# Optimization experiments

Hardware: AMD Instinct MI355X
Metric: run time of the kernel (lower is better)

Reference implementation:

```python
import jax, jax.numpy as jnp
import numpy as np

HASH_CODE_LEN = 8  # config['hash_code_len']
EPS = 1e-12

def _l2norm(x):
    n = jnp.sqrt(jnp.sum(x * x, axis=-1, keepdims=True))
    return x / jnp.maximum(n, EPS)

def setup_inputs() -> dict:
    key = jax.random.key(0)
    k1, k2, k3, k4 = jax.random.split(key, 4)
    B, H, S, D = 2, 12, 2048, 64
    Q = jax.random.normal(k1, (B, H, S, D), dtype=jnp.float32)
    K = jax.random.normal(k2, (B, H, S, D), dtype=jnp.float32)
    V = jax.random.normal(k3, (B, H, S, D), dtype=jnp.float32)
    mask = jnp.ones((B, S), dtype=jnp.float32)
    conv_w = jax.random.normal(k4, (H, 1, 3, 1), dtype=jnp.float32)  # depthwise Conv2d weight [H,1,w,1]
    return {"Q": Q, "K": K, "V": V, "mask": mask, "conv_w": conv_w}

def reference(Q, K, V, mask, conv_w):
    B, H, S, D = Q.shape
    # conv branch: depthwise conv over the sequence axis, per head (groups=num_head)
    Vm = V * mask[:, None, :, None]  # [B,H,S,D]
    conv_V = jax.lax.conv_general_dilated(
        Vm, conv_w,
        window_strides=(1, 1),
        padding=[(1, 1), (0, 0)],  # (conv_window//2, 0)
        dimension_numbers=("NCHW", "OIHW", "NCHW"),
        feature_group_count=H,
    )
    # YOSO attention: exact expectation of LSH cumulation.
    # collision prob of unit vectors q,k over hash_code_len bits: (1 - acos(q.k)/pi)^tau
    qn = _l2norm(Q)
    kn = _l2norm(K)
    dots = jnp.einsum("bhsd,bhtd->bhst", qn, kn)
    dots = jnp.clip(dots, -1.0, 1.0)
    W = (1.0 - jnp.arccos(dots) / jnp.pi) ** HASH_CODE_LEN  # [B,H,S,S]
    W = W * mask[:, None, None, :]  # key mask
    X = jnp.einsum("bhst,bhtd->bhsd", W, V)
    X = X * mask[:, None, :, None]  # query mask
    X = _l2norm(X)  # kernel.normalize(X)
    return X + conv_V
```

## Files before the change

### kernel.cpp

```cpp
#include <hip/hip_runtime.h>
#include <hip/hip_bf16.h>
#include <math.h>

#define NB 2
#define NH 12
#define NS 2048
#define ND 64
#define NBH (NB * NH)
#define TILE_USHORT 4096
#define QK_BLOCKS 6144
#define V_BLOCKS (NBH * 32)

typedef __attribute__((ext_vector_type(8))) short short8;
typedef __attribute__((ext_vector_type(4))) float floatx4;
typedef __attribute__((ext_vector_type(2))) float float2v;

__device__ __forceinline__ unsigned short f32_to_bf16_rne(float f) {
  unsigned int u = __float_as_uint(f);
  u += 0x7fffu + ((u >> 16) & 1u);
  return (unsigned short)(u >> 16);
}

__device__ __forceinline__ unsigned int pack_bf16_trunc(float lo, float hi) {
  return __builtin_amdgcn_perm(__float_as_uint(hi), __float_as_uint(lo), 0x07060302);
}

__device__ __forceinline__ float2v mk2(float x) { return (float2v){x, x}; }
__device__ __forceinline__ float2v max2(float2v a, float2v b) {
  return (float2v){fmaxf(a[0], b[0]), fmaxf(a[1], b[1])};
}
__device__ __forceinline__ float2v abs2(float2v a) {
  return (float2v){fabsf(a[0]), fabsf(a[1])};
}

__device__ __forceinline__ float yoso_f_exact(float d) {
  const float c0 = 0.49996030f;
  const float c1 = -0.06751822f;
  const float c2 = 0.02363774f;
  const float c3 = -0.00596174f;
  float a = fminf(fabsf(d), 1.0f);
  float p = fmaf(fmaf(fmaf(c3, a, c2), a, c1), a, c0);
  float u = sqrtf(1.0f - a) * p;
  return (d >= 0.0f) ? (1.0f - u) : u;
}

__global__ __launch_bounds__(256) void prep_all(
    const float* __restrict__ Q, const float* __restrict__ K,
    const float* __restrict__ V, const float* __restrict__ mask,
    unsigned short* __restrict__ qimg, unsigned short* __restrict__ kimg,
    unsigned short* __restrict__ vimg) {
  int blk = blockIdx.x;
  if (blk < QK_BLOCKS) {
    int row = blk * 16 + (threadIdx.x >> 4);
    int li  = threadIdx.x & 15;
    const float* src = Q;
    unsigned short* dst = qimg;
    if (row >= NBH * NS) { src = K; dst = kimg; row -= NBH * NS; }
    float4 v = *(const float4*)(src + (size_t)row * ND + li * 4);
    float ss = v.x * v.x + v.y * v.y + v.z * v.z + v.w * v.w;
    ss += __shfl_xor(ss, 1, 64);
    ss += __shfl_xor(ss, 2, 64);
    ss += __shfl_xor(ss, 4, 64);
    ss += __shfl_xor(ss, 8, 64);
    float rn = 1.0f / fmaxf(sqrtf(ss), 1e-12f);
    ushort4 o;
    o.x = f32_to_bf16_rne(v.x * rn);
    o.y = f32_to_bf16_rne(v.y * rn);
    o.z = f32_to_bf16_rne(v.z * rn);
    o.w = f32_to_bf16_rne(v.w * rn);
    int bh = row >> 11;
    int s  = row & (NS - 1);
    int kt = s >> 6, r = s & 63;
    int frag = (li >> 3) * 4 + (r >> 4);
    int ln   = ((li >> 1) & 3) * 16 + (r & 15);
    size_t off = (size_t)(bh * 32 + kt) * TILE_USHORT + frag * 512 + ln * 8 + (li & 1) * 4;
    *(ushort4*)(dst + off) = o;
  } else {
    int vb = blk - QK_BLOCKS;
    int bh = vb >> 5, kt = vb & 31, t0 = kt * 64;
    int b  = bh / NH;
    __shared__ float sT[64][65];
    int tid = threadIdx.x;
    int tr = tid >> 2;
    int dc = (tid & 3) * 16;
    float m = mask[b * NS + t0 + tr];
    const float* vp = V + ((size_t)bh * NS + t0 + tr) * ND + dc;
    #pragma unroll
    for (int jj = 0; jj < 16; jj += 4) {
      float4 v = *(const float4*)(vp + jj);
      sT[dc + jj + 0][tr] = v.x * m;
      sT[dc + jj + 1][tr] = v.y * m;
      sT[dc + jj + 2][tr] = v.z * m;
      sT[dc + jj + 3][tr] = v.w * m;
    }
    __syncthreads();
    int dr = tid >> 2;
    unsigned short* op = vimg + (size_t)(bh * 32 + kt) * TILE_USHORT;
    #pragma unroll
    for (int g = 0; g < 2; ++g) {
      int combo = (tid & 3) * 2 + g;
      int kk2 = combo >> 2;
      int qd  = combo & 3;
      uint4 u;
      int tb = kk2 * 32 + qd * 4;
      u.x = (unsigned int)f32_to_bf16_rne(sT[dr][tb + 0]) |
            ((unsigned int)f32_to_bf16_rne(sT[dr][tb + 1]) << 16);
      u.y = (unsigned int)f32_to_bf16_rne(sT[dr][tb + 2]) |
            ((unsigned int)f32_to_bf16_rne(sT[dr][tb + 3]) << 16);
      u.z = (unsigned int)f32_to_bf16_rne(sT[dr][tb + 16]) |
            ((unsigned int)f32_to_bf16_rne(sT[dr][tb + 17]) << 16);
      u.w = (unsigned int)f32_to_bf16_rne(sT[dr][tb + 18]) |
            ((unsigned int)f32_to_bf16_rne(sT[dr][tb + 19]) << 16);
      int frag = kk2 * 4 + (dr >> 4);
      int ln   = qd * 16 + (dr & 15);
      *(uint4*)(op + frag * 512 + ln * 8) = u;
    }
  }
}

__global__ __launch_bounds__(256, 3) void yoso_main(
    const unsigned short* __restrict__ qimg, const unsigned short* __restrict__ kimg,
    const unsigned short* __restrict__ vimg, const float* __restrict__ V,
    const float* __restrict__ mask, const float* __restrict__ conv_w,
    float* __restrict__ out) {
  int bh = blockIdx.x >> 5;
  int b  = bh / NH;
  int h  = bh % NH;
  int qt = blockIdx.x & 31;
  int s0 = qt * 64;

  __shared__ float xch[4 * 1088];

  int tid  = threadIdx.x;
  int wv   = tid >> 6;
  int lane = tid & 63;
  int lq   = lane & 15;
  int quad = lane >> 4;
  int qh   = wv & 1;
  int kp   = wv >> 1;

  uint4 qfrag[2][2];
  {
    const unsigned short* qtile = qimg + (size_t)(bh * 32 + qt) * TILE_USHORT;
    #pragma unroll
    for (int su = 0; su < 2; ++su)
      #pragma unroll
      for (int kk = 0; kk < 2; ++kk)
        qfrag[su][kk] = *(const uint4*)(qtile + (kk * 4 + qh * 2 + su) * 512 + lane * 8);
  }

  float w0 = conv_w[h * 3 + 0], w1 = conv_w[h * 3 + 1], w2 = conv_w[h * 3 + 2];

  floatx4 acc[2][4];
  #pragma unroll
  for (int su = 0; su < 2; ++su)
    #pragma unroll
    for (int fd = 0; fd < 4; ++fd) acc[su][fd] = (floatx4){0.f, 0.f, 0.f, 0.f};

  const unsigned short* kb  = kimg + (size_t)bh * 32 * TILE_USHORT;
  const unsigned short* vbI = vimg + (size_t)bh * 32 * TILE_USHORT;

  const float P0 = 0.3183098862f;
  const float P1 = 0.0530516477f;
  const float P2 = 0.0238732415f;
  const float P3 = 0.0142098402f;
  const float P4 = 0.0096701727f;
  const float P5 = 0.0071212906f;

  #pragma unroll 1
  for (int ss = 0; ss < 16; ++ss) {
    int kt = ss * 2 + kp;
    const unsigned short* ktile = kb  + (size_t)kt * TILE_USHORT;
    const unsigned short* vtile = vbI + (size_t)kt * TILE_USHORT;

    uint4 kf[2][4];
    #pragma unroll
    for (int kk = 0; kk < 2; ++kk)
      #pragma unroll
      for (int ft = 0; ft < 4; ++ft)
        kf[kk][ft] = *(const uint4*)(ktile + (kk * 4 + ft) * 512 + lane * 8);

    floatx4 sc[2][4];
    #pragma unroll
    for (int su = 0; su < 2; ++su)
      #pragma unroll
      for (int ft = 0; ft < 4; ++ft) sc[su][ft] = (floatx4){0.f, 0.f, 0.f, 0.f};
    #pragma unroll
    for (int kk = 0; kk < 2; ++kk)
      #pragma unroll
      for (int su = 0; su < 2; ++su) {
        short8 bq = *(const short8*)&qfrag[su][kk];
        #pragma unroll
        for (int ft = 0; ft < 4; ++ft)
          sc[su][ft] = __builtin_amdgcn_mfma_f32_16x16x32_bf16(
              *(const short8*)&kf[kk][ft], bq, sc[su][ft], 0, 0, 0);
      }

    uint4 vf[2][4];
    #pragma unroll
    for (int kk2 = 0; kk2 < 2; ++kk2)
      #pragma unroll
      for (int fd = 0; fd < 4; ++fd)
        vf[kk2][fd] = *(const uint4*)(vtile + (kk2 * 4 + fd) * 512 + lane * 8);

    {
      float2v mxy = mk2(0.f);
      #pragma unroll
      for (int su = 0; su < 2; ++su)
        #pragma unroll
        for (int ft = 0; ft < 4; ++ft) {
          float2v* p = (float2v*)&sc[su][ft];
          mxy = max2(mxy, max2(abs2(p[0]), abs2(p[1])));
        }
      float mx = fmaxf(mxy[0], mxy[1]);
      if (__builtin_expect(__any(mx > 0.82f), 0)) {
        #pragma unroll
        for (int su = 0; su < 2; ++su)
          #pragma unroll
          for (int ft = 0; ft < 4; ++ft)
            #pragma unroll
            for (int r = 0; r < 4; ++r) {
              float f = yoso_f_exact(sc[su][ft][r]);
              float f2 = f * f;
              float f4 = f2 * f2;
              sc[su][ft][r] = f4 * f4;
            }
      } else {
        float2v c5 = mk2(P5), c4 = mk2(P4), c3 = mk2(P3), c2 = mk2(P2),
                c1 = mk2(P1), c0 = mk2(P0), hf = mk2(0.5f);
        #pragma unroll
        for (int su = 0; su < 2; ++su)
          #pragma unroll
          for (int ft = 0; ft < 4; ++ft) {
            float2v* p = (float2v*)&sc[su][ft];
            #pragma unroll
            for (int hh = 0; hh < 2; ++hh) {
              float2v d = p[hh];
              float2v y = d * d;
              float2v pp = ((((c5 * y + c4) * y + c3) * y + c2) * y + c1) * y + c0;
              float2v f = pp * d + hf;
              float2v f2 = f * f;
              float2v f4 = f2 * f2;
              p[hh] = f4 * f4;
            }
          }
      }
    }

    #pragma unroll
    for (int kk2 = 0; kk2 < 2; ++kk2)
      #pragma unroll
      for (int su = 0; su < 2; ++su) {
        uint4 u;
        u.x = pack_bf16_trunc(sc[su][2 * kk2][0], sc[su][2 * kk2][1]);
        u.y = pack_bf16_trunc(sc[su][2 * kk2][2], sc[su][2 * kk2][3]);
        u.z = pack_bf16_trunc(sc[su][2 * kk2 + 1][0], sc[su][2 * kk2 + 1][1]);
        u.w = pack_bf16_trunc(sc[su][2 * kk2 + 1][2], sc[su][2 * kk2 + 1][3]);
        short8 bw = *(short8*)&u;
        #pragma unroll
        for (int fd = 0; fd < 4; ++fd)
          acc[su][fd] = __builtin_amdgcn_mfma_f32_16x16x32_bf16(
              *(const short8*)&vf[kk2][fd], bw, acc[su][fd], 0, 0, 0);
      }
  }

  __syncthreads();
  {
    float* wr = xch + wv * 1088;
    #pragma unroll
    for (int fd = 0; fd < 4; ++fd)
      #pragma unroll
      for (int r = 0; r < 4; ++r)
        wr[lq * 68 + fd * 16 + quad * 4 + r] = acc[1 - kp][fd][r];
  }
  __syncthreads();
  {
    const float* rd = xch + (wv ^ 2) * 1088;
    #pragma unroll
    for (int fd = 0; fd < 4; ++fd)
      #pragma unroll
      for (int r = 0; r < 4; ++r)
        acc[kp][fd][r] += rd[lq * 68 + fd * 16 + quad * 4 + r];
  }

  int s = s0 + qh * 32 + kp * 16 + lq;
  float qm  = mask[b * NS + s];
  float qm0 = (s > 0) ? mask[b * NS + s - 1] : 0.f;
  float qm2 = (s < NS - 1) ? mask[b * NS + s + 1] : 0.f;
  float ssum = 0.f;
  #pragma unroll
  for (int fd = 0; fd < 4; ++fd)
    #pragma unroll
    for (int r = 0; r < 4; ++r) {
      float x = acc[kp][fd][r] * qm;
      acc[kp][fd][r] = x;
      ssum += x * x;
    }
  ssum += __shfl_xor(ssum, 16, 64);
  ssum += __shfl_xor(ssum, 32, 64);
  float rn = 1.0f / fmaxf(sqrtf(ssum), 1e-12f);

  const float* vfull = V + ((size_t)bh * NS + s) * ND;
  #pragma unroll
  for (int fd = 0; fd < 4; ++fd) {
    int d = fd * 16 + quad * 4;
    float4 vc1 = *(const float4*)(vfull + d);
    float4 cv;
    cv.x = w1 * vc1.x * qm; cv.y = w1 * vc1.y * qm;
    cv.z = w1 * vc1.z * qm; cv.w = w1 * vc1.w * qm;
    if (s > 0) {
      float4 vc0 = *(const float4*)(vfull - ND + d);
      cv.x += w0 * vc0.x * qm0; cv.y += w0 * vc0.y * qm0;
      cv.z += w0 * vc0.z * qm0; cv.w += w0 * vc0.w * qm0;
    }
    if (s < NS - 1) {
      float4 vc2 = *(const float4*)(vfull + ND + d);
      cv.x += w2 * vc2.x * qm2; cv.y += w2 * vc2.y * qm2;
      cv.z += w2 * vc2.z * qm2; cv.w += w2 * vc2.w * qm2;
    }
    float4 o;
    o.x = acc[kp][fd][0] * rn + cv.x;
    o.y = acc[kp][fd][1] * rn + cv.y;
    o.z = acc[kp][fd][2] * rn + cv.z;
    o.w = acc[kp][fd][3] * rn + cv.w;
    *(float4*)(out + ((size_t)bh * NS + s) * ND + d) = o;
  }
}

extern "C" void kernel_launch(void* const* d_in, const int* in_sizes, int n_in,
                              void* d_out, int out_size, void* d_ws, size_t ws_size,
                              hipStream_t stream) {
  const float* Q      = (const float*)d_in[0];
  const float* K      = (const float*)d_in[1];
  const float* V      = (const float*)d_in[2];
  const float* mask   = (const float*)d_in[3];
  const float* conv_w = (const float*)d_in[4];
  float* out = (float*)d_out;

  const size_t seg = (size_t)NBH * NS * ND * sizeof(unsigned short);
  unsigned short* qimg = (unsigned short*)d_ws;
  unsigned short* kimg = (unsigned short*)((char*)d_ws + seg);
  unsigned short* vimg = (unsigned short*)((char*)d_ws + 2 * seg);

  prep_all<<<QK_BLOCKS + V_BLOCKS, 256, 0, stream>>>(Q, K, V, mask, qimg, kimg, vimg);
  yoso_main<<<NBH * 32, 256, 0, stream>>>(qimg, kimg, vimg, V, mask, conv_w, out);
}
```

Baseline: 151.3 us.

## Halve query tile per block to double grid size and raise occupancy

Each yoso_main block now handles 32 queries instead of 64, so twice as many blocks launch, and each wave computes a single 16-query sub-tile instead of two. Per-wave accumulators and score registers are halved, which allows launch bounds of 4 blocks per CU instead of 3 and a smaller shared exchange buffer. The cross-wave reduction becomes one-directional, with only half the waves doing the epilogue. The cost is that K and V tiles are reloaded twice as often per query, which doubles global and L2 traffic for K/V, and each loaded K/V fragment feeds half as many MFMAs.

```diff
diff --git a/kernel.cpp b/kernel.cpp
--- a/kernel.cpp
+++ b/kernel.cpp
@@ -118,44 +118,41 @@
   }
 }
 
-__global__ __launch_bounds__(256, 3) void yoso_main(
+__global__ __launch_bounds__(256, 4) void yoso_main(
     const unsigned short* __restrict__ qimg, const unsigned short* __restrict__ kimg,
     const unsigned short* __restrict__ vimg, const float* __restrict__ V,
     const float* __restrict__ mask, const float* __restrict__ conv_w,
     float* __restrict__ out) {
-  int bh = blockIdx.x >> 5;
+  int bh = blockIdx.x >> 6;
   int b  = bh / NH;
   int h  = bh % NH;
-  int qt = blockIdx.x & 31;
-  int s0 = qt * 64;
-
-  __shared__ float xch[4 * 1088];
+  int qt = blockIdx.x & 63;
+  int s0 = qt * 32;
+
+  __shared__ float xch[2 * 1088];
 
   int tid  = threadIdx.x;
   int wv   = tid >> 6;
   int lane = tid & 63;
   int lq   = lane & 15;
   int quad = lane >> 4;
-  int qh   = wv & 1;
+  int qs   = wv & 1;
   int kp   = wv >> 1;
 
-  uint4 qfrag[2][2];
+  uint4 qfrag[2];
   {
-    const unsigned short* qtile = qimg + (size_t)(bh * 32 + qt) * TILE_USHORT;
-    #pragma unroll
-    for (int su = 0; su < 2; ++su)
-      #pragma unroll
-      for (int kk = 0; kk < 2; ++kk)
-        qfrag[su][kk] = *(const uint4*)(qtile + (kk * 4 + qh * 2 + su) * 512 + lane * 8);
+    const unsigned short* qtile = qimg + (size_t)(bh * 32 + (qt >> 1)) * TILE_USHORT;
+    int nb = (qt & 1) * 2 + qs;
+    #pragma unroll
+    for (int kk = 0; kk < 2; ++kk)
+      qfrag[kk] = *(const uint4*)(qtile + (kk * 4 + nb) * 512 + lane * 8);
   }
 
   float w0 = conv_w[h * 3 + 0], w1 = conv_w[h * 3 + 1], w2 = conv_w[h * 3 + 2];
 
-  floatx4 acc[2][4];
+  floatx4 acc[4];
   #pragma unroll
-  for (int su = 0; su < 2; ++su)
-    #pragma unroll
-    for (int fd = 0; fd < 4; ++fd) acc[su][fd] = (floatx4){0.f, 0.f, 0.f, 0.f};
+  for (int fd = 0; fd < 4; ++fd) acc[fd] = (floatx4){0.f, 0.f, 0.f, 0.f};
 
   const unsigned short* kb  = kimg + (size_t)bh * 32 * TILE_USHORT;
   const unsigned short* vbI = vimg + (size_t)bh * 32 * TILE_USHORT;
@@ -180,21 +177,17 @@
       for (int ft = 0; ft < 4; ++ft)
         kf[kk][ft] = *(const uint4*)(ktile + (kk * 4 + ft) * 512 + lane * 8);
 
-    floatx4 sc[2][4];
-    #pragma unroll
-    for (int su = 0; su < 2; ++su)
-      #pragma unroll
-      for (int ft = 0; ft < 4; ++ft) sc[su][ft] = (floatx4){0.f, 0.f, 0.f, 0.f};
-    #pragma unroll
-    for (int kk = 0; kk < 2; ++kk)
-      #pragma unroll
-      for (int su = 0; su < 2; ++su) {
-        short8 bq = *(const short8*)&qfrag[su][kk];
-        #pragma unroll
-        for (int ft = 0; ft < 4; ++ft)
-          sc[su][ft] = __builtin_amdgcn_mfma_f32_16x16x32_bf16(
-              *(const short8*)&kf[kk][ft], bq, sc[su][ft], 0, 0, 0);
-      }
+    floatx4 sc[4];
+    #pragma unroll
+    for (int ft = 0; ft < 4; ++ft) sc[ft] = (floatx4){0.f, 0.f, 0.f, 0.f};
+    #pragma unroll
+    for (int kk = 0; kk < 2; ++kk) {
+      short8 bq = *(const short8*)&qfrag[kk];
+      #pragma unroll
+      for (int ft = 0; ft < 4; ++ft)
+        sc[ft] = __builtin_amdgcn_mfma_f32_16x16x32_bf16(
+            *(const short8*)&kf[kk][ft], bq, sc[ft], 0, 0, 0);
+    }
 
     uint4 vf[2][4];
     #pragma unroll
@@ -206,124 +199,115 @@
     {
       float2v mxy = mk2(0.f);
       #pragma unroll
-      for (int su = 0; su < 2; ++su)
-        #pragma unroll
-        for (int ft = 0; ft < 4; ++ft) {
-          float2v* p = (float2v*)&sc[su][ft];
-          mxy = max2(mxy, max2(abs2(p[0]), abs2(p[1])));
-        }
+      for (int ft = 0; ft < 4; ++ft) {
+        float2v* p = (float2v*)&sc[ft];
+        mxy = max2(mxy, max2(abs2(p[0]), abs2(p[1])));
+      }
       float mx = fmaxf(mxy[0], mxy[1]);
       if (__builtin_expect(__any(mx > 0.82f), 0)) {
         #pragma unroll
-        for (int su = 0; su < 2; ++su)
+        for (int ft = 0; ft < 4; ++ft)
           #pragma unroll
-          for (int ft = 0; ft < 4; ++ft)
-            #pragma unroll
-            for (int r = 0; r < 4; ++r) {
-              float f = yoso_f_exact(sc[su][ft][r]);
-              float f2 = f * f;
-              float f4 = f2 * f2;
-              sc[su][ft][r] = f4 * f4;
-            }
+          for (int r = 0; r < 4; ++r) {
+            float f = yoso_f_exact(sc[ft][r]);
+            float f2 = f * f;
+            float f4 = f2 * f2;
+            sc[ft][r] = f4 * f4;
+          }
       } else {
         float2v c5 = mk2(P5), c4 = mk2(P4), c3 = mk2(P3), c2 = mk2(P2),
                 c1 = mk2(P1), c0 = mk2(P0), hf = mk2(0.5f);
         #pragma unroll
-        for (int su = 0; su < 2; ++su)
+        for (int ft = 0; ft < 4; ++ft) {
+          float2v* p = (float2v*)&sc[ft];
           #pragma unroll
-          for (int ft = 0; ft < 4; ++ft) {
-            float2v* p = (float2v*)&sc[su][ft];
-            #pragma unroll
-            for (int hh = 0; hh < 2; ++hh) {
-              float2v d = p[hh];
-              float2v y = d * d;
-              float2v pp = ((((c5 * y + c4) * y + c3) * y + c2) * y + c1) * y + c0;
-              float2v f = pp * d + hf;
-              float2v f2 = f * f;
-              float2v f4 = f2 * f2;
-              p[hh] = f4 * f4;
-            }
+          for (int hh = 0; hh < 2; ++hh) {
+            float2v d = p[hh];
+            float2v y = d * d;
+            float2v pp = ((((c5 * y + c4) * y + c3) * y + c2) * y + c1) * y + c0;
+            float2v f = pp * d + hf;
+            float2v f2 = f * f;
+            float2v f4 = f2 * f2;
+            p[hh] = f4 * f4;
           }
-      }
-    }
-
-    #pragma unroll
-    for (int kk2 = 0; kk2 < 2; ++kk2)
-      #pragma unroll
-      for (int su = 0; su < 2; ++su) {
-        uint4 u;
-        u.x = pack_bf16_trunc(sc[su][2 * kk2][0], sc[su][2 * kk2][1]);
-        u.y = pack_bf16_trunc(sc[su][2 * kk2][2], sc[su][2 * kk2][3]);
-        u.z = pack_bf16_trunc(sc[su][2 * kk2 + 1][0], sc[su][2 * kk2 + 1][1]);
-        u.w = pack_bf16_trunc(sc[su][2 * kk2 + 1][2], sc[su][2 * kk2 + 1][3]);
-        short8 bw = *(short8*)&u;
-        #pragma unroll
-        for (int fd = 0; fd < 4; ++fd)
-          acc[su][fd] = __builtin_amdgcn_mfma_f32_16x16x32_bf16(
-              *(const short8*)&vf[kk2][fd], bw, acc[su][fd], 0, 0, 0);
-      }
-  }
-
+        }
+      }
+    }
+
+    #pragma unroll
+    for (int kk2 = 0; kk2 < 2; ++kk2) {
+      uint4 u;
+      u.x = pack_bf16_trunc(sc[2 * kk2][0], sc[2 * kk2][1]);
+      u.y = pack_bf16_trunc(sc[2 * kk2][2], sc[2 * kk2][3]);
+      u.z = pack_bf16_trunc(sc[2 * kk2 + 1][0], sc[2 * kk2 + 1][1]);
+      u.w = pack_bf16_trunc(sc[2 * kk2 + 1][2], sc[2 * kk2 + 1][3]);
+      short8 bw = *(short8*)&u;
+      #pragma unroll
+      for (int fd = 0; fd < 4; ++fd)
+        acc[fd] = __builtin_amdgcn_mfma_f32_16x16x32_bf16(
+            *(const short8*)&vf[kk2][fd], bw, acc[fd], 0, 0, 0);
+    }
+  }
+
+  if (kp == 1) {
+    float* wr = xch + qs * 1088;
+    #pragma unroll
+    for (int fd = 0; fd < 4; ++fd)
+      #pragma unroll
+      for (int r = 0; r < 4; ++r)
+        wr[lq * 68 + fd * 16 + quad * 4 + r] = acc[fd][r];
+  }
   __syncthreads();
-  {
-    float* wr = xch + wv * 1088;
+  if (kp == 0) {
+    const float* rd = xch + qs * 1088;
     #pragma unroll
     for (int fd = 0; fd < 4; ++fd)
       #pragma unroll
       for (int r = 0; r < 4; ++r)
-        wr[lq * 68 + fd * 16 + quad * 4 + r] = acc[1 - kp][fd][r];
-  }
-  __syncthreads();
-  {
-    const float* rd = xch + (wv ^ 2) * 1088;
+        acc[fd][r] += rd[lq * 68 + fd * 16 + quad * 4 + r];
+
+    int s = s0 + qs * 16 + lq;
+    float qm  = mask[b * NS + s];
+    float qm0 = (s > 0) ? mask[b * NS + s - 1] : 0.f;
+    float qm2 = (s < NS - 1) ? mask[b * NS + s + 1] : 0.f;
+    float ssum = 0.f;
     #pragma unroll
     for (int fd = 0; fd < 4; ++fd)
       #pragma unroll
-      for (int r = 0; r < 4; ++r)
-        acc[kp][fd][r] += rd[lq * 68 + fd * 16 + quad * 4 + r];
-  }
-
-  int s = s0 + qh * 32 + kp * 16 + lq;
-  float qm  = mask[b * NS + s];
-  float qm0 = (s > 0) ? mask[b * NS + s - 1] : 0.f;
-  float qm2 = (s < NS - 1) ? mask[b * NS + s + 1] : 0.f;
-  float ssum = 0.f;
-  #pragma unroll
-  for (int fd = 0; fd < 4; ++fd)
-    #pragma unroll
-    for (int r = 0; r < 4; ++r) {
-      float x = acc[kp][fd][r] * qm;
-      acc[kp][fd][r] = x;
-      ssum += x * x;
-    }
-  ssum += __shfl_xor(ssum, 16, 64);
-  ssum += __shfl_xor(ssum, 32, 64);
-  float rn = 1.0f / fmaxf(sqrtf(ssum), 1e-12f);
-
-  const float* vfull = V + ((size_t)bh * NS + s) * ND;
-  #pragma unroll
-  for (int fd = 0; fd < 4; ++fd) {
-    int d = fd * 16 + quad * 4;
-    float4 vc1 = *(const float4*)(vfull + d);
-    float4 cv;
-    cv.x = w1 * vc1.x * qm; cv.y = w1 * vc1.y * qm;
-    cv.z = w1 * vc1.z * qm; cv.w = w1 * vc1.w * qm;
-    if (s > 0) {
-      float4 vc0 = *(const float4*)(vfull - ND + d);
-      cv.x += w0 * vc0.x * qm0; cv.y += w0 * vc0.y * qm0;
-      cv.z += w0 * vc0.z * qm0; cv.w += w0 * vc0.w * qm0;
-    }
-    if (s < NS - 1) {
-      float4 vc2 = *(const float4*)(vfull + ND + d);
-      cv.x += w2 * vc2.x * qm2; cv.y += w2 * vc2.y * qm2;
-      cv.z += w2 * vc2.z * qm2; cv.w += w2 * vc2.w * qm2;
-    }
-    float4 o;
-    o.x = acc[kp][fd][0] * rn + cv.x;
-    o.y = acc[kp][fd][1] * rn + cv.y;
-    o.z = acc[kp][fd][2] * rn + cv.z;
-    o.w = acc[kp][fd][3] * rn + cv.w;
-    *(float4*)(out + ((size_t)bh * NS + s) * ND + d) = o;
+      for (int r = 0; r < 4; ++r) {
+        float x = acc[fd][r] * qm;
+        acc[fd][r] = x;
+        ssum += x * x;
+      }
+    ssum += __shfl_xor(ssum, 16, 64);
+    ssum += __shfl_xor(ssum, 32, 64);
+    float rn = 1.0f / fmaxf(sqrtf(ssum), 1e-12f);
+
+    const float* vfull = V + ((size_t)bh * NS + s) * ND;
+    #pragma unroll
+    for (int fd = 0; fd < 4; ++fd) {
+      int d = fd * 16 + quad * 4;
+      float4 vc1 = *(const float4*)(vfull + d);
+      float4 cv;
+      cv.x = w1 * vc1.x * qm; cv.y = w1 * vc1.y * qm;
+      cv.z = w1 * vc1.z * qm; cv.w = w1 * vc1.w * qm;
+      if (s > 0) {
+        float4 vc0 = *(const float4*)(vfull - ND + d);
+        cv.x += w0 * vc0.x * qm0; cv.y += w0 * vc0.y * qm0;
+        cv.z += w0 * vc0.z * qm0; cv.w += w0 * vc0.w * qm0;
+      }
+      if (s < NS - 1) {
+        float4 vc2 = *(const float4*)(vfull + ND + d);
+        cv.x += w2 * vc2.x * qm2; cv.y += w2 * vc2.y * qm2;
+        cv.z += w2 * vc2.z * qm2; cv.w += w2 * vc2.w * qm2;
+      }
+      float4 o;
+      o.x = acc[fd][0] * rn + cv.x;
+      o.y = acc[fd][1] * rn + cv.y;
+      o.z = acc[fd][2] * rn + cv.z;
+      o.w = acc[fd][3] * rn + cv.w;
+      *(float4*)(out + ((size_t)bh * NS + s) * ND + d) = o;
+    }
   }
 }
 
@@ -343,5 +327,5 @@
   unsigned short* vimg = (unsigned short*)((char*)d_ws + 2 * seg);
 
   prep_all<<<QK_BLOCKS + V_BLOCKS, 256, 0, stream>>>(Q, K, V, mask, qimg, kimg, vimg);
-  yoso_main<<<NBH * 32, 256, 0, stream>>>(qimg, kimg, vimg, V, mask, conv_w, out);
-}
+  yoso_main<<<NBH * 64, 256, 0, stream>>>(qimg, kimg, vimg, V, mask, conv_w, out);
+}
```

Result: faster. 146.4 us (-3.2%).

## Split key range across two blocks and reduce partials in finalize kernel

Applied to the files above, without the earlier changes.

The main attention kernel now splits the key tiles into two halves, so twice as many blocks run (1536 instead of 768), and launch bounds rise to 6 blocks per CU. Each half writes its unnormalized partial sum as bf16 to a workspace buffer. A new finalize kernel adds the two partials, applies the query mask and L2 normalisation, and adds the depthwise conv branch. This targets poor occupancy and wave count on a GPU with many CUs, at the cost of an extra kernel launch, extra global traffic for the partials, and bf16 rounding of the partial sums.

```diff
diff --git a/kernel.cpp b/kernel.cpp
--- a/kernel.cpp
+++ b/kernel.cpp
@@ -31,6 +31,10 @@
 }
 __device__ __forceinline__ float2v abs2(float2v a) {
   return (float2v){fabsf(a[0]), fabsf(a[1])};
+}
+
+__device__ __forceinline__ float bf16_to_f32(unsigned short u) {
+  return __uint_as_float((unsigned int)u << 16);
 }
 
 __device__ __forceinline__ float yoso_f_exact(float d) {
@@ -118,15 +122,13 @@
   }
 }
 
-__global__ __launch_bounds__(256, 3) void yoso_main(
+__global__ __launch_bounds__(256, 6) void yoso_main(
     const unsigned short* __restrict__ qimg, const unsigned short* __restrict__ kimg,
-    const unsigned short* __restrict__ vimg, const float* __restrict__ V,
-    const float* __restrict__ mask, const float* __restrict__ conv_w,
-    float* __restrict__ out) {
-  int bh = blockIdx.x >> 5;
-  int b  = bh / NH;
-  int h  = bh % NH;
-  int qt = blockIdx.x & 31;
+    const unsigned short* __restrict__ vimg,
+    unsigned short* __restrict__ parts) {
+  int bh = blockIdx.x >> 6;
+  int qt = (blockIdx.x >> 1) & 31;
+  int kh = blockIdx.x & 1;
   int s0 = qt * 64;
 
   __shared__ float xch[4 * 1088];
@@ -149,8 +151,6 @@
         qfrag[su][kk] = *(const uint4*)(qtile + (kk * 4 + qh * 2 + su) * 512 + lane * 8);
   }
 
-  float w0 = conv_w[h * 3 + 0], w1 = conv_w[h * 3 + 1], w2 = conv_w[h * 3 + 2];
-
   floatx4 acc[2][4];
   #pragma unroll
   for (int su = 0; su < 2; ++su)
@@ -168,8 +168,8 @@
   const float P5 = 0.0071212906f;
 
   #pragma unroll 1
-  for (int ss = 0; ss < 16; ++ss) {
-    int kt = ss * 2 + kp;
+  for (int ss = 0; ss < 8; ++ss) {
+    int kt = kh * 16 + ss * 2 + kp;
     const unsigned short* ktile = kb  + (size_t)kt * TILE_USHORT;
     const unsigned short* vtile = vbI + (size_t)kt * TILE_USHORT;
 
@@ -284,47 +284,67 @@
   }
 
   int s = s0 + qh * 32 + kp * 16 + lq;
-  float qm  = mask[b * NS + s];
-  float qm0 = (s > 0) ? mask[b * NS + s - 1] : 0.f;
-  float qm2 = (s < NS - 1) ? mask[b * NS + s + 1] : 0.f;
-  float ssum = 0.f;
-  #pragma unroll
-  for (int fd = 0; fd < 4; ++fd)
-    #pragma unroll
-    for (int r = 0; r < 4; ++r) {
-      float x = acc[kp][fd][r] * qm;
-      acc[kp][fd][r] = x;
-      ssum += x * x;
-    }
-  ssum += __shfl_xor(ssum, 16, 64);
-  ssum += __shfl_xor(ssum, 32, 64);
-  float rn = 1.0f / fmaxf(sqrtf(ssum), 1e-12f);
-
-  const float* vfull = V + ((size_t)bh * NS + s) * ND;
+  unsigned short* pp = parts + (size_t)kh * NBH * NS * ND + ((size_t)bh * NS + s) * ND;
   #pragma unroll
   for (int fd = 0; fd < 4; ++fd) {
     int d = fd * 16 + quad * 4;
-    float4 vc1 = *(const float4*)(vfull + d);
-    float4 cv;
-    cv.x = w1 * vc1.x * qm; cv.y = w1 * vc1.y * qm;
-    cv.z = w1 * vc1.z * qm; cv.w = w1 * vc1.w * qm;
-    if (s > 0) {
-      float4 vc0 = *(const float4*)(vfull - ND + d);
-      cv.x += w0 * vc0.x * qm0; cv.y += w0 * vc0.y * qm0;
-      cv.z += w0 * vc0.z * qm0; cv.w += w0 * vc0.w * qm0;
-    }
-    if (s < NS - 1) {
-      float4 vc2 = *(const float4*)(vfull + ND + d);
-      cv.x += w2 * vc2.x * qm2; cv.y += w2 * vc2.y * qm2;
-      cv.z += w2 * vc2.z * qm2; cv.w += w2 * vc2.w * qm2;
-    }
-    float4 o;
-    o.x = acc[kp][fd][0] * rn + cv.x;
-    o.y = acc[kp][fd][1] * rn + cv.y;
-    o.z = acc[kp][fd][2] * rn + cv.z;
-    o.w = acc[kp][fd][3] * rn + cv.w;
-    *(float4*)(out + ((size_t)bh * NS + s) * ND + d) = o;
-  }
+    uint2 o;
+    o.x = (unsigned int)f32_to_bf16_rne(acc[kp][fd][0]) |
+          ((unsigned int)f32_to_bf16_rne(acc[kp][fd][1]) << 16);
+    o.y = (unsigned int)f32_to_bf16_rne(acc[kp][fd][2]) |
+          ((unsigned int)f32_to_bf16_rne(acc[kp][fd][3]) << 16);
+    *(uint2*)(pp + d) = o;
+  }
+}
+
+__global__ __launch_bounds__(256) void yoso_finalize(
+    const unsigned short* __restrict__ parts, const float* __restrict__ V,
+    const float* __restrict__ mask, const float* __restrict__ conv_w,
+    float* __restrict__ out) {
+  int row = blockIdx.x * 16 + (threadIdx.x >> 4);
+  int li  = threadIdx.x & 15;
+  int bh = row >> 11;
+  int s  = row & (NS - 1);
+  int b = bh / NH, h = bh % NH;
+
+  size_t base = (size_t)row * ND + li * 4;
+  ushort4 ua = *(const ushort4*)(parts + base);
+  ushort4 ub = *(const ushort4*)(parts + (size_t)NBH * NS * ND + base);
+  float qm = mask[b * NS + s];
+  float x0 = (bf16_to_f32(ua.x) + bf16_to_f32(ub.x)) * qm;
+  float x1 = (bf16_to_f32(ua.y) + bf16_to_f32(ub.y)) * qm;
+  float x2 = (bf16_to_f32(ua.z) + bf16_to_f32(ub.z)) * qm;
+  float x3 = (bf16_to_f32(ua.w) + bf16_to_f32(ub.w)) * qm;
+  float ss = x0 * x0 + x1 * x1 + x2 * x2 + x3 * x3;
+  ss += __shfl_xor(ss, 1, 64);
+  ss += __shfl_xor(ss, 2, 64);
+  ss += __shfl_xor(ss, 4, 64);
+  ss += __shfl_xor(ss, 8, 64);
+  float rn = 1.0f / fmaxf(sqrtf(ss), 1e-12f);
+
+  float w0 = conv_w[h * 3 + 0], w1 = conv_w[h * 3 + 1], w2 = conv_w[h * 3 + 2];
+  float4 v1 = *(const float4*)(V + base);
+  float4 cv;
+  cv.x = w1 * v1.x * qm; cv.y = w1 * v1.y * qm;
+  cv.z = w1 * v1.z * qm; cv.w = w1 * v1.w * qm;
+  if (s > 0) {
+    float qm0 = mask[b * NS + s - 1];
+    float4 v0 = *(const float4*)(V + base - ND);
+    cv.x += w0 * v0.x * qm0; cv.y += w0 * v0.y * qm0;
+    cv.z += w0 * v0.z * qm0; cv.w += w0 * v0.w * qm0;
+  }
+  if (s < NS - 1) {
+    float qm2 = mask[b * NS + s + 1];
+    float4 v2 = *(const float4*)(V + base + ND);
+    cv.x += w2 * v2.x * qm2; cv.y += w2 * v2.y * qm2;
+    cv.z += w2 * v2.z * qm2; cv.w += w2 * v2.w * qm2;
+  }
+  float4 o;
+  o.x = x0 * rn + cv.x;
+  o.y = x1 * rn + cv.y;
+  o.z = x2 * rn + cv.z;
+  o.w = x3 * rn + cv.w;
+  *(float4*)(out + base) = o;
 }
 
 extern "C" void kernel_launch(void* const* d_in, const int* in_sizes, int n_in,
@@ -338,10 +358,12 @@
   float* out = (float*)d_out;
 
   const size_t seg = (size_t)NBH * NS * ND * sizeof(unsigned short);
-  unsigned short* qimg = (unsigned short*)d_ws;
-  unsigned short* kimg = (unsigned short*)((char*)d_ws + seg);
-  unsigned short* vimg = (unsigned short*)((char*)d_ws + 2 * seg);
+  unsigned short* qimg  = (unsigned short*)d_ws;
+  unsigned short* kimg  = (unsigned short*)((char*)d_ws + seg);
+  unsigned short* vimg  = (unsigned short*)((char*)d_ws + 2 * seg);
+  unsigned short* parts = (unsigned short*)((char*)d_ws + 3 * seg);
 
   prep_all<<<QK_BLOCKS + V_BLOCKS, 256, 0, stream>>>(Q, K, V, mask, qimg, kimg, vimg);
-  yoso_main<<<NBH * 32, 256, 0, stream>>>(qimg, kimg, vimg, V, mask, conv_w, out);
-}
+  yoso_main<<<NBH * 64, 256, 0, stream>>>(qimg, kimg, vimg, parts);
+  yoso_finalize<<<NBH * NS / 16, 256, 0, stream>>>(parts, V, mask, conv_w, out);
+}
```

New measurement: 286.8 us. 1.9x slower.
